# Optimization experiments

Hardware: AMD Instinct MI355X
Metric: run time of the kernel (lower is better)

Reference implementation:

```python
import jax, jax.numpy as jnp
import numpy as np

B, T, D, H = 8, 2048, 1024, 128  # batch, seq, input_size, head_size


def setup_inputs() -> dict:
    key = jax.random.key(0)
    kx, kq, kk, kv = jax.random.split(key, 4)
    s = 1.0 / np.sqrt(D)
    return {
        "x": jax.random.normal(kx, (B, T, D), dtype=jnp.float32),
        "Wq": jax.random.normal(kq, (D, H), dtype=jnp.float32) * s,
        "Wk": jax.random.normal(kk, (D, H), dtype=jnp.float32) * s,
        "Wv": jax.random.normal(kv, (D, H), dtype=jnp.float32) * s,
    }


def reference(x, Wq, Wk, Wv):
    # projections (Linear, no bias)
    q = jnp.einsum("btd,dh->bth", x, Wq)
    k = jnp.einsum("btd,dh->bth", x, Wk)
    v = jnp.einsum("btd,dh->bth", x, Wv)
    scale = H ** (-0.5)
    scores = jnp.einsum("bth,bsh->bts", q, k) * scale  # [B,T,T]
    t = x.shape[1]
    causal = jnp.tril(jnp.ones((t, t), dtype=bool))
    scores = jnp.where(causal, scores, -jnp.inf)
    attn = jax.nn.softmax(scores, axis=-1)  # dropout p=0.0 -> identity
    out = jnp.einsum("bts,bsh->bth", attn, v)
    return out
```

## Files before the change

kernel.cpp:

```cpp
#include <hip/hip_runtime.h>
#include <math.h>

#define B_ 8
#define T_ 2048
#define D_ 1024
#define H_ 128
#define BT (B_ * T_)

typedef short bf16x8 __attribute__((ext_vector_type(8)));
typedef float f32x4 __attribute__((ext_vector_type(4)));

static constexpr float SCALE = 0.08838834764831845f;

__device__ inline unsigned short f2b(float f) {
  unsigned int u = __float_as_uint(f);
  u += 0x7FFF + ((u >> 16) & 1);
  return (unsigned short)(u >> 16);
}
__device__ inline unsigned int pk2(float a, float b) {
  return (unsigned int)f2b(a) | ((unsigned int)f2b(b) << 16);
}

__device__ __forceinline__ void gll16(const void* g, void* l) {
  __builtin_amdgcn_global_load_lds(
      (const __attribute__((address_space(1))) void*)g,
      (__attribute__((address_space(3))) void*)l, 16, 0, 0);
}

__global__ __launch_bounds__(256) void wcvt_kernel(
    const float* __restrict__ Wq, const float* __restrict__ Wk,
    const float* __restrict__ Wv, short* __restrict__ Wt) {
  __shared__ short Wls[128 * 72];
  const int sel = blockIdx.y;
  const float* W = sel == 0 ? Wq : (sel == 1 ? Wk : Wv);
  const int d0 = blockIdx.x * 64;
  const int tid = threadIdx.x;
#pragma unroll
  for (int i = 0; i < 8; ++i) {
    int slot = tid + i * 256;
    int r = slot >> 5, hg = slot & 31;
    float4 w = *(const float4*)(W + (size_t)(d0 + r) * H_ + hg * 4);
    Wls[(hg * 4 + 0) * 72 + r] = (short)f2b(w.x);
    Wls[(hg * 4 + 1) * 72 + r] = (short)f2b(w.y);
    Wls[(hg * 4 + 2) * 72 + r] = (short)f2b(w.z);
    Wls[(hg * 4 + 3) * 72 + r] = (short)f2b(w.w);
  }
  __syncthreads();
  short* dst = Wt + (size_t)sel * D_ * H_;
#pragma unroll
  for (int i = 0; i < 4; ++i) {
    int slot = tid + i * 256;
    int h = slot >> 3, g = slot & 7;
    *(int4*)(dst + (size_t)h * D_ + d0 + g * 8) = *(int4*)&Wls[h * 72 + g * 8];
  }
}

__global__ __launch_bounds__(256) void proj_kernel(
    const float* __restrict__ x, const short* __restrict__ Wt,
    short* __restrict__ qb, short* __restrict__ kb, short* __restrict__ vtb) {
  __shared__ alignas(16) char smem[36864];
  short* Xs = (short*)smem;
  short* Ws = (short*)(smem + 16384);

  const int tid = threadIdx.x;
  const int wave = tid >> 6, lane = tid & 63;
  const int ln = lane & 15, quad = lane >> 4;
  const int mw = wave & 1, nw = wave >> 1;
  const int sel = blockIdx.y;
  const int row0 = blockIdx.x * 128;
  const short* W = Wt + (size_t)sel * (size_t)(D_ * H_);

  f32x4 acc[4][4];
#pragma unroll
  for (int mi = 0; mi < 4; ++mi)
#pragma unroll
    for (int ni = 0; ni < 4; ++ni) acc[mi][ni] = (f32x4){0.f, 0.f, 0.f, 0.f};

  for (int s = 0; s < 16; ++s) {
    const int k0 = s * 64;
    if (s) __syncthreads();

#pragma unroll
    for (int j = 0; j < 4; ++j) {
      const int rbase = wave * 32 + j * 8;
      const int n = rbase + (lane >> 3);
      const int gp = (lane & 7) ^ (n & 7);
      gll16(W + (size_t)n * D_ + k0 + gp * 8, (char*)Ws + rbase * 128);
    }
    {
      float4 xr[8];
#pragma unroll
      for (int i = 0; i < 8; ++i) {
        int fid = tid + i * 256;
        int r = fid >> 4, g4 = fid & 15;
        xr[i] = *(const float4*)(x + (size_t)(row0 + r) * D_ + k0 + g4 * 4);
      }
#pragma unroll
      for (int i = 0; i < 8; ++i) {
        int fid = tid + i * 256;
        int r = fid >> 4, g4 = fid & 15;
        int g = g4 >> 1, half = g4 & 1;
        unsigned int* p = (unsigned int*)&Xs[r * 64 + ((g ^ (r & 7)) * 8) + half * 4];
        p[0] = pk2(xr[i].x, xr[i].y);
        p[1] = pk2(xr[i].z, xr[i].w);
      }
    }
    __syncthreads();

#pragma unroll
    for (int kk = 0; kk < 2; ++kk) {
      bf16x8 a[4];
#pragma unroll
      for (int mi = 0; mi < 4; ++mi) {
        int r = mw * 64 + mi * 16 + ln;
        int g = kk * 4 + quad;
        a[mi] = *(bf16x8*)&Xs[r * 64 + ((g ^ (r & 7)) * 8)];
      }
#pragma unroll
      for (int ni = 0; ni < 4; ++ni) {
        int n = nw * 64 + ni * 16 + ln;
        int g = kk * 4 + quad;
        bf16x8 bb = *(bf16x8*)&Ws[n * 64 + ((g ^ (n & 7)) * 8)];
#pragma unroll
        for (int mi = 0; mi < 4; ++mi)
          acc[mi][ni] = __builtin_amdgcn_mfma_f32_16x16x32_bf16(a[mi], bb, acc[mi][ni], 0, 0, 0);
      }
    }
  }

  __syncthreads();
  short* Cs = (short*)smem;
  if (sel < 2) {
    short* out = sel ? kb : qb;
#pragma unroll
    for (int mi = 0; mi < 4; ++mi)
#pragma unroll
      for (int ni = 0; ni < 4; ++ni)
#pragma unroll
        for (int rr = 0; rr < 4; ++rr)
          Cs[(mw * 64 + mi * 16 + quad * 4 + rr) * 136 + nw * 64 + ni * 16 + ln] =
              (short)f2b(acc[mi][ni][rr]);
    __syncthreads();
#pragma unroll
    for (int i = 0; i < 8; ++i) {
      int slot = tid + i * 256;
      int r = slot >> 4, g = slot & 15;
      *(int4*)(out + (size_t)(row0 + r) * H_ + g * 8) = *(int4*)&Cs[r * 136 + g * 8];
    }
  } else {
#pragma unroll
    for (int mi = 0; mi < 4; ++mi)
#pragma unroll
      for (int ni = 0; ni < 4; ++ni)
#pragma unroll
        for (int rr = 0; rr < 4; ++rr)
          Cs[(nw * 64 + ni * 16 + ln) * 136 + mw * 64 + mi * 16 + quad * 4 + rr] =
              (short)f2b(acc[mi][ni][rr]);
    __syncthreads();
    const int b = row0 >> 11, t0 = row0 & 2047;
#pragma unroll
    for (int i = 0; i < 8; ++i) {
      int slot = tid + i * 256;
      int h = slot >> 4, g = slot & 15;
      *(int4*)(vtb + (size_t)(b * H_ + h) * T_ + t0 + g * 8) = *(int4*)&Cs[h * 136 + g * 8];
    }
  }
}

__global__ __launch_bounds__(128) void attn_kernel(
    const short* __restrict__ qb, const short* __restrict__ kb,
    const short* __restrict__ vtb, float* __restrict__ out) {
  __shared__ alignas(16) char smem[53632];
  short* Ks0 = (short*)smem;
  short* Ks1 = (short*)(smem + 16384);
  short* Vt  = (short*)(smem + 32768);
  short* Pt  = (short*)(smem + 49152);

  const int tid = threadIdx.x;
  const int wv = tid >> 6, lane = tid & 63;
  const int ln = lane & 15, quad = lane >> 4;
  const int slot = blockIdx.x & 255;
  const int pass = blockIdx.x >> 8;
  const int b = slot >> 5;
  const int j = slot & 31;
  const int tile = pass ? (63 - j) : j;
  const int q0 = tile * 32;

  short* myP = Pt + wv * (16 * 68);

  bf16x8 qfr[4];
#pragma unroll
  for (int kk = 0; kk < 4; ++kk)
    qfr[kk] = *(const bf16x8*)(qb + (size_t)(b * T_ + q0 + wv * 16 + ln) * H_ +
                               kk * 32 + quad * 8);

  f32x4 oacc[8];
#pragma unroll
  for (int ht = 0; ht < 8; ++ht) oacc[ht] = (f32x4){0.f, 0.f, 0.f, 0.f};

  float m_run = -INFINITY, l_run = 0.f;
  const int qglob = q0 + wv * 16 + ln;

  auto stageK = [&](short* dst, int s0) {
#pragma unroll
    for (int jj = 0; jj < 8; ++jj) {
      const int rb = wv * 32 + jj * 4;
      const int r = rb + (lane >> 4);
      const int gp = (lane & 15) ^ (r & 7);
      gll16(kb + (size_t)(b * T_ + s0 + r) * H_ + gp * 8, (char*)dst + rb * 256);
    }
  };
  auto stageV = [&](int s0) {
#pragma unroll
    for (int jj = 0; jj < 8; ++jj) {
      const int hb = wv * 64 + jj * 8;
      const int h = hb + (lane >> 3);
      const int gp = (lane & 7) ^ (h & 7);
      gll16(vtb + (size_t)(b * H_ + h) * T_ + s0 + gp * 8, (char*)Vt + hb * 128);
    }
  };

  const int nch = (q0 >> 6) + 1;
  stageK(Ks0, 0);

  for (int ch = 0; ch < nch; ++ch) {
    const int s0 = ch * 64;
    short* Kc = (ch & 1) ? Ks1 : Ks0;
    __syncthreads();
    stageV(s0);
    if (ch + 1 < nch) stageK((ch & 1) ? Ks0 : Ks1, s0 + 64);

    f32x4 sacc[4];
#pragma unroll
    for (int t = 0; t < 4; ++t) sacc[t] = (f32x4){0.f, 0.f, 0.f, 0.f};
#pragma unroll
    for (int kk = 0; kk < 4; ++kk) {
#pragma unroll
      for (int t = 0; t < 4; ++t) {
        const int krow = t * 16 + ln;
        bf16x8 kf = *(bf16x8*)&Kc[krow * 128 + (((kk * 4 + quad) ^ (ln & 7)) * 8)];
        sacc[t] = __builtin_amdgcn_mfma_f32_16x16x32_bf16(kf, qfr[kk], sacc[t], 0, 0, 0);
      }
    }

    float sv[4][4];
    float mc = -INFINITY;
#pragma unroll
    for (int t = 0; t < 4; ++t)
#pragma unroll
      for (int r = 0; r < 4; ++r) {
        const int key = s0 + t * 16 + quad * 4 + r;
        float s = sacc[t][r] * SCALE;
        sv[t][r] = (key <= qglob) ? s : -INFINITY;
        mc = fmaxf(mc, sv[t][r]);
      }
    mc = fmaxf(mc, __shfl_xor(mc, 16));
    mc = fmaxf(mc, __shfl_xor(mc, 32));
    const float mnew = fmaxf(m_run, mc);
    const float alpha = __expf(m_run - mnew);
    float lc = 0.f;
    float p[4][4];
#pragma unroll
    for (int t = 0; t < 4; ++t)
#pragma unroll
      for (int r = 0; r < 4; ++r) {
        p[t][r] = __expf(sv[t][r] - mnew);
        lc += p[t][r];
      }
    lc += __shfl_xor(lc, 16);
    lc += __shfl_xor(lc, 32);
    l_run = l_run * alpha + lc;
    m_run = mnew;

#pragma unroll
    for (int t = 0; t < 4; ++t) {
      *(unsigned int*)&myP[ln * 68 + t * 16 + quad * 4 + 0] = pk2(p[t][0], p[t][1]);
      *(unsigned int*)&myP[ln * 68 + t * 16 + quad * 4 + 2] = pk2(p[t][2], p[t][3]);
    }
#pragma unroll
    for (int ht = 0; ht < 8; ++ht)
#pragma unroll
      for (int r = 0; r < 4; ++r) oacc[ht][r] *= alpha;

    __syncthreads();

#pragma unroll
    for (int kk2 = 0; kk2 < 2; ++kk2) {
      bf16x8 pf = *(bf16x8*)&myP[ln * 68 + kk2 * 32 + quad * 8];
#pragma unroll
      for (int ht = 0; ht < 8; ++ht) {
        const int hrow = ht * 16 + ln;
        bf16x8 vf = *(bf16x8*)&Vt[hrow * 64 + (((kk2 * 4 + quad) ^ (ln & 7)) * 8)];
        oacc[ht] = __builtin_amdgcn_mfma_f32_16x16x32_bf16(vf, pf, oacc[ht], 0, 0, 0);
      }
    }
  }

  const float linv = 1.0f / l_run;
#pragma unroll
  for (int ht = 0; ht < 8; ++ht)
#pragma unroll
    for (int r = 0; r < 4; ++r) oacc[ht][r] *= linv;

  __syncthreads();
  float* Ot = (float*)smem;
#pragma unroll
  for (int ht = 0; ht < 8; ++ht) {
    double2* dst = (double2*)&Ot[(wv * 16 + ln) * 132 + ht * 16 + quad * 4];
    *(double2*)dst = *(double2*)&oacc[ht];
  }
  __syncthreads();
#pragma unroll
  for (int i = 0; i < 8; ++i) {
    int slot2 = tid + i * 128;
    int r = slot2 >> 5, c = slot2 & 31;
    float4 v = *(float4*)&Ot[r * 132 + c * 4];
    *(float4*)(out + (size_t)(b * T_ + q0 + r) * H_ + c * 4) = v;
  }
}

extern "C" void kernel_launch(void* const* d_in, const int* in_sizes, int n_in,
                              void* d_out, int out_size, void* d_ws, size_t ws_size,
                              hipStream_t stream) {
  const float* x  = (const float*)d_in[0];
  const float* Wq = (const float*)d_in[1];
  const float* Wk = (const float*)d_in[2];
  const float* Wv = (const float*)d_in[3];
  float* out = (float*)d_out;

  char* ws = (char*)d_ws;
  short* qb  = (short*)(ws);
  short* kb  = (short*)(ws + 4194304);
  short* vtb = (short*)(ws + 8388608);
  short* Wt  = (short*)(ws + 12582912);

  wcvt_kernel<<<dim3(D_ / 64, 3), 256, 0, stream>>>(Wq, Wk, Wv, Wt);
  proj_kernel<<<dim3(BT / 128, 3), 256, 0, stream>>>(x, Wt, qb, kb, vtb);
  attn_kernel<<<dim3(512), 128, 0, stream>>>(qb, kb, vtb, out);
}
```

Baseline: 176.6 us.

## Double-buffer projection and V tiles, halve projection row tile

The projection kernel now uses 64-row tiles (twice as many blocks) and double-buffers X and W in shared memory, prefetching the next K slice while the current one is computed. The attention kernel double-buffers V alongside K, prefetching the next chunk, and drops one barrier per chunk. The goal is to overlap global loads with MFMA work and to raise occupancy and parallelism for the projection. The cost is more LDS per block (about 68 KB for attention), which may cut concurrent blocks per CU, and each W slice is read by more projection blocks.

```diff
diff --git a/kernel.cpp b/kernel.cpp
--- a/kernel.cpp
+++ b/kernel.cpp
@@ -58,28 +58,28 @@
 __global__ __launch_bounds__(256) void proj_kernel(
     const float* __restrict__ x, const short* __restrict__ Wt,
     short* __restrict__ qb, short* __restrict__ kb, short* __restrict__ vtb) {
-  __shared__ alignas(16) char smem[36864];
-  short* Xs = (short*)smem;
-  short* Ws = (short*)(smem + 16384);
+  __shared__ alignas(16) char smem[49152];
+  short* Xs0 = (short*)smem;
+  short* Xs1 = (short*)(smem + 8192);
+  short* Ws0 = (short*)(smem + 16384);
+  short* Ws1 = (short*)(smem + 32768);
 
   const int tid = threadIdx.x;
   const int wave = tid >> 6, lane = tid & 63;
   const int ln = lane & 15, quad = lane >> 4;
   const int mw = wave & 1, nw = wave >> 1;
   const int sel = blockIdx.y;
-  const int row0 = blockIdx.x * 128;
+  const int row0 = blockIdx.x * 64;
   const short* W = Wt + (size_t)sel * (size_t)(D_ * H_);
 
-  f32x4 acc[4][4];
-#pragma unroll
-  for (int mi = 0; mi < 4; ++mi)
+  f32x4 acc[2][4];
+#pragma unroll
+  for (int mi = 0; mi < 2; ++mi)
 #pragma unroll
     for (int ni = 0; ni < 4; ++ni) acc[mi][ni] = (f32x4){0.f, 0.f, 0.f, 0.f};
 
-  for (int s = 0; s < 16; ++s) {
-    const int k0 = s * 64;
-    if (s) __syncthreads();
-
+  auto stage = [&](int bf, int k0) {
+    short* Ws = bf ? Ws1 : Ws0;
 #pragma unroll
     for (int j = 0; j < 4; ++j) {
       const int rbase = wave * 32 + j * 8;
@@ -87,42 +87,45 @@
       const int gp = (lane & 7) ^ (n & 7);
       gll16(W + (size_t)n * D_ + k0 + gp * 8, (char*)Ws + rbase * 128);
     }
-    {
-      float4 xr[8];
-#pragma unroll
-      for (int i = 0; i < 8; ++i) {
-        int fid = tid + i * 256;
-        int r = fid >> 4, g4 = fid & 15;
-        xr[i] = *(const float4*)(x + (size_t)(row0 + r) * D_ + k0 + g4 * 4);
-      }
-#pragma unroll
-      for (int i = 0; i < 8; ++i) {
-        int fid = tid + i * 256;
-        int r = fid >> 4, g4 = fid & 15;
-        int g = g4 >> 1, half = g4 & 1;
-        unsigned int* p = (unsigned int*)&Xs[r * 64 + ((g ^ (r & 7)) * 8) + half * 4];
-        p[0] = pk2(xr[i].x, xr[i].y);
-        p[1] = pk2(xr[i].z, xr[i].w);
-      }
-    }
+    short* Xs = bf ? Xs1 : Xs0;
+    float4 xr[4];
+#pragma unroll
+    for (int i = 0; i < 4; ++i) {
+      int fid = tid + i * 256;
+      int r = fid >> 4, g4 = fid & 15;
+      xr[i] = *(const float4*)(x + (size_t)(row0 + r) * D_ + k0 + g4 * 4);
+    }
+#pragma unroll
+    for (int i = 0; i < 4; ++i) {
+      int fid = tid + i * 256;
+      int r = fid >> 4, g4 = fid & 15;
+      int g = g4 >> 1, half = g4 & 1;
+      unsigned int* p = (unsigned int*)&Xs[r * 64 + ((g ^ (r & 7)) * 8) + half * 4];
+      p[0] = pk2(xr[i].x, xr[i].y);
+      p[1] = pk2(xr[i].z, xr[i].w);
+    }
+  };
+
+  stage(0, 0);
+  for (int s = 0; s < 16; ++s) {
     __syncthreads();
-
+    if (s < 15) stage((s + 1) & 1, (s + 1) * 64);
+    const short* Xs = (s & 1) ? Xs1 : Xs0;
+    const short* Ws = (s & 1) ? Ws1 : Ws0;
 #pragma unroll
     for (int kk = 0; kk < 2; ++kk) {
-      bf16x8 a[4];
-#pragma unroll
-      for (int mi = 0; mi < 4; ++mi) {
-        int r = mw * 64 + mi * 16 + ln;
-        int g = kk * 4 + quad;
-        a[mi] = *(bf16x8*)&Xs[r * 64 + ((g ^ (r & 7)) * 8)];
+      bf16x8 a[2];
+#pragma unroll
+      for (int mi = 0; mi < 2; ++mi) {
+        int r = mw * 32 + mi * 16 + ln;
+        a[mi] = *(bf16x8*)&Xs[r * 64 + (((kk * 4 + quad) ^ (r & 7)) * 8)];
       }
 #pragma unroll
       for (int ni = 0; ni < 4; ++ni) {
         int n = nw * 64 + ni * 16 + ln;
-        int g = kk * 4 + quad;
-        bf16x8 bb = *(bf16x8*)&Ws[n * 64 + ((g ^ (n & 7)) * 8)];
-#pragma unroll
-        for (int mi = 0; mi < 4; ++mi)
+        bf16x8 bb = *(bf16x8*)&Ws[n * 64 + (((kk * 4 + quad) ^ (n & 7)) * 8)];
+#pragma unroll
+        for (int mi = 0; mi < 2; ++mi)
           acc[mi][ni] = __builtin_amdgcn_mfma_f32_16x16x32_bf16(a[mi], bb, acc[mi][ni], 0, 0, 0);
       }
     }
@@ -133,36 +136,36 @@
   if (sel < 2) {
     short* out = sel ? kb : qb;
 #pragma unroll
-    for (int mi = 0; mi < 4; ++mi)
+    for (int mi = 0; mi < 2; ++mi)
 #pragma unroll
       for (int ni = 0; ni < 4; ++ni)
 #pragma unroll
         for (int rr = 0; rr < 4; ++rr)
-          Cs[(mw * 64 + mi * 16 + quad * 4 + rr) * 136 + nw * 64 + ni * 16 + ln] =
+          Cs[(mw * 32 + mi * 16 + quad * 4 + rr) * 136 + nw * 64 + ni * 16 + ln] =
               (short)f2b(acc[mi][ni][rr]);
     __syncthreads();
 #pragma unroll
-    for (int i = 0; i < 8; ++i) {
+    for (int i = 0; i < 4; ++i) {
       int slot = tid + i * 256;
       int r = slot >> 4, g = slot & 15;
       *(int4*)(out + (size_t)(row0 + r) * H_ + g * 8) = *(int4*)&Cs[r * 136 + g * 8];
     }
   } else {
 #pragma unroll
-    for (int mi = 0; mi < 4; ++mi)
+    for (int mi = 0; mi < 2; ++mi)
 #pragma unroll
       for (int ni = 0; ni < 4; ++ni)
 #pragma unroll
         for (int rr = 0; rr < 4; ++rr)
-          Cs[(nw * 64 + ni * 16 + ln) * 136 + mw * 64 + mi * 16 + quad * 4 + rr] =
+          Cs[(nw * 64 + ni * 16 + ln) * 72 + mw * 32 + mi * 16 + quad * 4 + rr] =
               (short)f2b(acc[mi][ni][rr]);
     __syncthreads();
     const int b = row0 >> 11, t0 = row0 & 2047;
 #pragma unroll
-    for (int i = 0; i < 8; ++i) {
+    for (int i = 0; i < 4; ++i) {
       int slot = tid + i * 256;
-      int h = slot >> 4, g = slot & 15;
-      *(int4*)(vtb + (size_t)(b * H_ + h) * T_ + t0 + g * 8) = *(int4*)&Cs[h * 136 + g * 8];
+      int h = slot >> 3, g = slot & 7;
+      *(int4*)(vtb + (size_t)(b * H_ + h) * T_ + t0 + g * 8) = *(int4*)&Cs[h * 72 + g * 8];
     }
   }
 }
@@ -170,11 +173,12 @@
 __global__ __launch_bounds__(128) void attn_kernel(
     const short* __restrict__ qb, const short* __restrict__ kb,
     const short* __restrict__ vtb, float* __restrict__ out) {
-  __shared__ alignas(16) char smem[53632];
+  __shared__ alignas(16) char smem[69888];
   short* Ks0 = (short*)smem;
   short* Ks1 = (short*)(smem + 16384);
-  short* Vt  = (short*)(smem + 32768);
-  short* Pt  = (short*)(smem + 49152);
+  short* Vt0 = (short*)(smem + 32768);
+  short* Vt1 = (short*)(smem + 49152);
+  short* Pt  = (short*)(smem + 65536);
 
   const int tid = threadIdx.x;
   const int wv = tid >> 6, lane = tid & 63;
@@ -210,25 +214,30 @@
       gll16(kb + (size_t)(b * T_ + s0 + r) * H_ + gp * 8, (char*)dst + rb * 256);
     }
   };
-  auto stageV = [&](int s0) {
+  auto stageV = [&](short* dst, int s0) {
 #pragma unroll
     for (int jj = 0; jj < 8; ++jj) {
       const int hb = wv * 64 + jj * 8;
       const int h = hb + (lane >> 3);
       const int gp = (lane & 7) ^ (h & 7);
-      gll16(vtb + (size_t)(b * H_ + h) * T_ + s0 + gp * 8, (char*)Vt + hb * 128);
+      gll16(vtb + (size_t)(b * H_ + h) * T_ + s0 + gp * 8, (char*)dst + hb * 128);
     }
   };
 
   const int nch = (q0 >> 6) + 1;
   stageK(Ks0, 0);
+  stageV(Vt0, 0);
 
   for (int ch = 0; ch < nch; ++ch) {
     const int s0 = ch * 64;
-    short* Kc = (ch & 1) ? Ks1 : Ks0;
+    const int cur = ch & 1;
     __syncthreads();
-    stageV(s0);
-    if (ch + 1 < nch) stageK((ch & 1) ? Ks0 : Ks1, s0 + 64);
+    if (ch + 1 < nch) {
+      stageK(cur ? Ks0 : Ks1, s0 + 64);
+      stageV(cur ? Vt0 : Vt1, s0 + 64);
+    }
+    const short* Kc = cur ? Ks1 : Ks0;
+    const short* Vc = cur ? Vt1 : Vt0;
 
     f32x4 sacc[4];
 #pragma unroll
@@ -282,15 +291,13 @@
 #pragma unroll
       for (int r = 0; r < 4; ++r) oacc[ht][r] *= alpha;
 
-    __syncthreads();
-
 #pragma unroll
     for (int kk2 = 0; kk2 < 2; ++kk2) {
       bf16x8 pf = *(bf16x8*)&myP[ln * 68 + kk2 * 32 + quad * 8];
 #pragma unroll
       for (int ht = 0; ht < 8; ++ht) {
         const int hrow = ht * 16 + ln;
-        bf16x8 vf = *(bf16x8*)&Vt[hrow * 64 + (((kk2 * 4 + quad) ^ (ln & 7)) * 8)];
+        bf16x8 vf = *(bf16x8*)&Vc[hrow * 64 + (((kk2 * 4 + quad) ^ (ln & 7)) * 8)];
         oacc[ht] = __builtin_amdgcn_mfma_f32_16x16x32_bf16(vf, pf, oacc[ht], 0, 0, 0);
       }
     }
@@ -305,10 +312,8 @@
   __syncthreads();
   float* Ot = (float*)smem;
 #pragma unroll
-  for (int ht = 0; ht < 8; ++ht) {
-    double2* dst = (double2*)&Ot[(wv * 16 + ln) * 132 + ht * 16 + quad * 4];
-    *(double2*)dst = *(double2*)&oacc[ht];
-  }
+  for (int ht = 0; ht < 8; ++ht)
+    *(f32x4*)&Ot[(wv * 16 + ln) * 132 + ht * 16 + quad * 4] = oacc[ht];
   __syncthreads();
 #pragma unroll
   for (int i = 0; i < 8; ++i) {
@@ -335,6 +340,6 @@
   short* Wt  = (short*)(ws + 12582912);
 
   wcvt_kernel<<<dim3(D_ / 64, 3), 256, 0, stream>>>(Wq, Wk, Wv, Wt);
-  proj_kernel<<<dim3(BT / 128, 3), 256, 0, stream>>>(x, Wt, qb, kb, vtb);
+  proj_kernel<<<dim3(BT / 64, 3), 256, 0, stream>>>(x, Wt, qb, kb, vtb);
   attn_kernel<<<dim3(512), 128, 0, stream>>>(qb, kb, vtb, out);
 }
```

After: 172.4 us. 1.02x faster.
